# Kernel tuning notes

Measured on AMD Instinct MI355X. Metric: run time of the kernel, lower is better.

## Reference

```python
import jax, jax.numpy as jnp
import numpy as np

EMBED = 1024
HEADS = 16
HEAD_DIM = EMBED // HEADS


def setup_inputs() -> dict:
    key = jax.random.key(0)
    ks = jax.random.split(key, 8)
    N, S = 4, 2048
    scale = 1.0 / np.sqrt(HEAD_DIM)
    return {
        "values": jax.random.normal(ks[0], (N, S, EMBED), jnp.float32),
        "keys": jax.random.normal(ks[1], (N, S, EMBED), jnp.float32),
        "query": jax.random.normal(ks[2], (N, S, EMBED), jnp.float32),
        "Wv": jax.random.normal(ks[3], (HEAD_DIM, HEAD_DIM), jnp.float32) * scale,
        "Wk": jax.random.normal(ks[4], (HEAD_DIM, HEAD_DIM), jnp.float32) * scale,
        "Wq": jax.random.normal(ks[5], (HEAD_DIM, HEAD_DIM), jnp.float32) * scale,
        "Wo": jax.random.normal(ks[6], (EMBED, EMBED), jnp.float32) / np.sqrt(EMBED),
        "bo": jax.random.normal(ks[7], (EMBED,), jnp.float32) * 0.01,
    }


def reference(values, keys, query, Wv, Wk, Wq, Wo, bo):
    N = query.shape[0]
    # reshape to [N, S, H, D]
    v = values.reshape(N, -1, HEADS, HEAD_DIM)
    k = keys.reshape(N, -1, HEADS, HEAD_DIM)
    q = query.reshape(N, -1, HEADS, HEAD_DIM)
    # per-head linear projections (torch Linear: x @ W.T)
    v = jnp.einsum("nshd,ed->nshe", v, Wv)
    k = jnp.einsum("nshd,ed->nshe", k, Wk)
    q = jnp.einsum("nshd,ed->nshe", q, Wq)
    # full attention matrix [N, H, Q, K]; note scale uses embed_size**0.5 as in source
    energy = jnp.einsum("nqhd,nkhd->nhqk", q, k)
    attn = jax.nn.softmax(energy / jnp.sqrt(jnp.asarray(EMBED, energy.dtype)), axis=3)
    out = jnp.einsum("nhql,nlhd->nqhd", attn, v).reshape(N, -1, EMBED)
    return out @ Wo.T + bo
```

## Files before the change

kernel.cpp:

```cpp
#include <hip/hip_runtime.h>
#include <hip/hip_bf16.h>

#define EMBED 1024
#define HEADS 16
#define HD    64
#define NB    4
#define SEQ   2048

typedef __bf16 bf16x8 __attribute__((ext_vector_type(8)));
typedef float  f32x4  __attribute__((ext_vector_type(4)));

__device__ __forceinline__ unsigned short f2bf(float f) {
    union { float f; unsigned u; } v; v.f = f;
    unsigned r = v.u + 0x7fffu + ((v.u >> 16) & 1u);
    return (unsigned short)(r >> 16);
}

__global__ __launch_bounds__(256) void cvt_kernel(const float* __restrict__ src,
                                                  unsigned short* __restrict__ dst) {
    int i = blockIdx.x * 256 + threadIdx.x;
    float4 v = ((const float4*)src)[i];
    ushort4 o;
    o.x = f2bf(v.x); o.y = f2bf(v.y); o.z = f2bf(v.z); o.w = f2bf(v.w);
    ((ushort4*)dst)[i] = o;
}

__global__ __launch_bounds__(256) void proj_kernel(
    const float* __restrict__ xq, const float* __restrict__ xk, const float* __restrict__ xv,
    const float* __restrict__ Wq, const float* __restrict__ Wk, const float* __restrict__ Wv,
    unsigned short* __restrict__ Qp, unsigned short* __restrict__ Kp, unsigned short* __restrict__ Vt)
{
    __shared__ __align__(16) unsigned short Wl[64 * 72];
    __shared__ __align__(16) unsigned short Xl[128 * 72];

    int bx = blockIdx.x;
    int p  = bx >> 10;
    int r  = bx & 1023;
    int st = r & 15, h = (r >> 4) & 15, n = r >> 8;
    int s0 = st * 128;

    const float* x = (p == 0) ? xq : (p == 1) ? xk : xv;
    const float* W = (p == 0) ? Wq : (p == 1) ? Wk : Wv;
    const float sc = (p == 0) ? 0.045084220027780106f : 1.0f;

    int tid = threadIdx.x;

    for (int i = 0; i < 4; ++i) {
        int idx = tid + i * 256;
        int row = idx >> 4, c4 = idx & 15;
        float4 wv = ((const float4*)W)[row * 16 + c4];
        int o = row * 72 + c4 * 4;
        Wl[o] = f2bf(wv.x); Wl[o+1] = f2bf(wv.y); Wl[o+2] = f2bf(wv.z); Wl[o+3] = f2bf(wv.w);
    }
    const float* xbase = x + (size_t)(n * SEQ + s0) * EMBED + h * HD;
    for (int i = 0; i < 8; ++i) {
        int idx = tid + i * 256;
        int row = idx >> 4, c4 = idx & 15;
        float4 v = *(const float4*)(xbase + (size_t)row * EMBED + c4 * 4);
        int o = row * 72 + c4 * 4;
        Xl[o] = f2bf(v.x); Xl[o+1] = f2bf(v.y); Xl[o+2] = f2bf(v.z); Xl[o+3] = f2bf(v.w);
    }
    __syncthreads();

    int w = tid >> 6, lane = tid & 63, ln = lane & 15, qd = lane >> 4;

    bf16x8 a[2][2], b[4][2];
    for (int mt = 0; mt < 2; ++mt)
        for (int kt = 0; kt < 2; ++kt)
            a[mt][kt] = *(const bf16x8*)&Xl[(w * 32 + mt * 16 + ln) * 72 + kt * 32 + qd * 8];
    for (int nt = 0; nt < 4; ++nt)
        for (int kt = 0; kt < 2; ++kt)
            b[nt][kt] = *(const bf16x8*)&Wl[(nt * 16 + ln) * 72 + kt * 32 + qd * 8];

    f32x4 acc[2][4];
    const f32x4 fz = {0.f, 0.f, 0.f, 0.f};
    for (int mt = 0; mt < 2; ++mt) for (int nt = 0; nt < 4; ++nt) acc[mt][nt] = fz;
    for (int mt = 0; mt < 2; ++mt)
        for (int nt = 0; nt < 4; ++nt) {
            acc[mt][nt] = __builtin_amdgcn_mfma_f32_16x16x32_bf16(a[mt][0], b[nt][0], acc[mt][nt], 0, 0, 0);
            acc[mt][nt] = __builtin_amdgcn_mfma_f32_16x16x32_bf16(a[mt][1], b[nt][1], acc[mt][nt], 0, 0, 0);
        }
    __syncthreads();

    if (p < 2) {
        for (int mt = 0; mt < 2; ++mt)
            for (int nt = 0; nt < 4; ++nt)
                for (int rg = 0; rg < 4; ++rg)
                    Xl[(w * 32 + mt * 16 + qd * 4 + rg) * 72 + nt * 16 + ln] = f2bf(acc[mt][nt][rg] * sc);
        __syncthreads();
        unsigned short* outp = (p == 0 ? Qp : Kp) + (size_t)(n * HEADS + h) * SEQ * HD + (size_t)s0 * HD;
        for (int i = 0; i < 4; ++i) {
            int idx = tid + i * 256;
            int row = idx >> 3, ch = idx & 7;
            *(uint4*)(outp + (size_t)row * HD + ch * 8) = *(const uint4*)&Xl[row * 72 + ch * 8];
        }
    } else {
        for (int mt = 0; mt < 2; ++mt)
            for (int nt = 0; nt < 4; ++nt)
                for (int rg = 0; rg < 4; ++rg)
                    Xl[(nt * 16 + ln) * 136 + (w * 32 + mt * 16 + qd * 4 + rg)] = f2bf(acc[mt][nt][rg]);
        __syncthreads();
        unsigned short* outp = Vt + (size_t)(n * HEADS + h) * HD * SEQ + s0;
        for (int i = 0; i < 4; ++i) {
            int idx = tid + i * 256;
            int row = idx >> 4, ch = idx & 15;
            *(uint4*)(outp + (size_t)row * SEQ + ch * 8) = *(const uint4*)&Xl[row * 136 + ch * 8];
        }
    }
}

__global__ __launch_bounds__(256) void attn_kernel(
    const unsigned short* __restrict__ Qp, const unsigned short* __restrict__ Kp,
    const unsigned short* __restrict__ Vt, unsigned short* __restrict__ Xattn)
{
    __shared__ __align__(16) unsigned short Kl[64 * 72];
    __shared__ __align__(16) unsigned short Vl[64 * 72];
    __shared__ __align__(16) unsigned short Pl[128 * 72];

    int bx = blockIdx.x;
    int head = bx >> 4, qt = bx & 15;
    int n = head >> 4, h = head & 15;
    int q0 = qt * 128;

    int tid = threadIdx.x;
    int w = tid >> 6, lane = tid & 63, ln = lane & 15, qd = lane >> 4;

    const unsigned short* Qb = Qp + (size_t)head * SEQ * HD;
    const unsigned short* Kb = Kp + (size_t)head * SEQ * HD;
    const unsigned short* Vb = Vt + (size_t)head * HD * SEQ;

    bf16x8 qa[2][2];
    for (int mt = 0; mt < 2; ++mt)
        for (int kt = 0; kt < 2; ++kt)
            qa[mt][kt] = *(const bf16x8*)(Qb + (size_t)(q0 + w * 32 + mt * 16 + ln) * HD + kt * 32 + qd * 8);

    const f32x4 fz = {0.f, 0.f, 0.f, 0.f};
    f32x4 o[2][4];
    float lp[2][4];
    for (int mt = 0; mt < 2; ++mt)
        for (int nt = 0; nt < 4; ++nt) o[mt][nt] = fz;
    for (int mt = 0; mt < 2; ++mt)
        for (int rg = 0; rg < 4; ++rg) lp[mt][rg] = 0.f;

    int wsw = (qd & 2) << 3;
    int rsw = (ln & 8) << 1;

    for (int kc = 0; kc < SEQ; kc += 64) {
        for (int i = 0; i < 2; ++i) {
            int idx = tid + i * 256;
            int row = idx >> 3, ch = idx & 7;
            uint4 kv = *(const uint4*)(Kb + (size_t)(kc + row) * HD + ch * 8);
            uint4 vv = *(const uint4*)(Vb + (size_t)row * SEQ + kc + ch * 8);
            *(uint4*)&Kl[row * 72 + ch * 8] = kv;
            *(uint4*)&Vl[row * 72 + ch * 8] = vv;
        }
        __syncthreads();

        bf16x8 kb[4][2];
        for (int nt = 0; nt < 4; ++nt)
            for (int kt = 0; kt < 2; ++kt)
                kb[nt][kt] = *(const bf16x8*)&Kl[(nt * 16 + ln) * 72 + kt * 32 + qd * 8];
        f32x4 s[2][4];
        for (int mt = 0; mt < 2; ++mt)
            for (int nt = 0; nt < 4; ++nt) {
                f32x4 acc = fz;
                acc = __builtin_amdgcn_mfma_f32_16x16x32_bf16(qa[mt][0], kb[nt][0], acc, 0, 0, 0);
                acc = __builtin_amdgcn_mfma_f32_16x16x32_bf16(qa[mt][1], kb[nt][1], acc, 0, 0, 0);
                s[mt][nt] = acc;
            }

        for (int mt = 0; mt < 2; ++mt)
            for (int nt = 0; nt < 4; ++nt) {
                int colsw = (nt * 16 + ln) ^ wsw;
#pragma unroll
                for (int rg = 0; rg < 4; ++rg) {
                    float p = __builtin_amdgcn_exp2f(s[mt][nt][rg]);
                    lp[mt][rg] += p;
                    union { float f; unsigned u; } c; c.f = p;
                    Pl[(w * 32 + mt * 16 + qd * 4 + rg) * 72 + colsw] =
                        (unsigned short)((c.u + 0x8000u) >> 16);
                }
            }
        __asm__ volatile("s_waitcnt lgkmcnt(0)" ::: "memory");

        bf16x8 pa[2][2], vf[4][2];
        for (int mt = 0; mt < 2; ++mt)
            for (int kt = 0; kt < 2; ++kt)
                pa[mt][kt] = *(const bf16x8*)&Pl[(w * 32 + mt * 16 + ln) * 72 + ((kt * 32 + qd * 8) ^ rsw)];
        for (int nt = 0; nt < 4; ++nt)
            for (int kt = 0; kt < 2; ++kt)
                vf[nt][kt] = *(const bf16x8*)&Vl[(nt * 16 + ln) * 72 + kt * 32 + qd * 8];
        for (int mt = 0; mt < 2; ++mt)
            for (int nt = 0; nt < 4; ++nt) {
                o[mt][nt] = __builtin_amdgcn_mfma_f32_16x16x32_bf16(pa[mt][0], vf[nt][0], o[mt][nt], 0, 0, 0);
                o[mt][nt] = __builtin_amdgcn_mfma_f32_16x16x32_bf16(pa[mt][1], vf[nt][1], o[mt][nt], 0, 0, 0);
            }
        __syncthreads();
    }

    for (int mt = 0; mt < 2; ++mt)
        for (int rg = 0; rg < 4; ++rg) {
            float v = lp[mt][rg];
            for (int d = 1; d < 16; d <<= 1) v += __shfl_xor(v, d);
            lp[mt][rg] = 1.0f / v;
        }

    for (int mt = 0; mt < 2; ++mt)
        for (int nt = 0; nt < 4; ++nt)
            for (int rg = 0; rg < 4; ++rg)
                Pl[(w * 32 + mt * 16 + qd * 4 + rg) * 72 + nt * 16 + ln] = f2bf(o[mt][nt][rg] * lp[mt][rg]);
    __syncthreads();
    unsigned short* ob = Xattn + (size_t)(n * SEQ + q0) * EMBED + h * HD;
    for (int i = 0; i < 4; ++i) {
        int idx = tid + i * 256;
        int row = idx >> 3, ch = idx & 7;
        *(uint4*)(ob + (size_t)row * EMBED + ch * 8) = *(const uint4*)&Pl[row * 72 + ch * 8];
    }
}

__global__ __launch_bounds__(256) void outproj_kernel(
    const unsigned short* __restrict__ X, const unsigned short* __restrict__ Wb,
    const float* __restrict__ bo, float* __restrict__ out)
{
    __shared__ __align__(16) unsigned short Al[128 * 72];
    __shared__ __align__(16) unsigned short Bl[128 * 72];

    int bx = blockIdx.x;
    int cm = bx >> 3, cn = bx & 7;
    int m0 = cm * 128, c0 = cn * 128;
    int tid = threadIdx.x;
    int w = tid >> 6, lane = tid & 63, ln = lane & 15, qd = lane >> 4;
    int rh = (w & 1) * 64, chh = (w >> 1) * 64;

    f32x4 acc[4][4];
    const f32x4 fz = {0.f, 0.f, 0.f, 0.f};
    for (int mt = 0; mt < 4; ++mt) for (int nt = 0; nt < 4; ++nt) acc[mt][nt] = fz;

    for (int k0 = 0; k0 < EMBED; k0 += 64) {
        for (int i = 0; i < 4; ++i) {
            int idx = tid + i * 256;
            int row = idx >> 3, ch = idx & 7;
            uint4 av = *(const uint4*)(X  + (size_t)(m0 + row) * EMBED + k0 + ch * 8);
            uint4 bv = *(const uint4*)(Wb + (size_t)(c0 + row) * EMBED + k0 + ch * 8);
            *(uint4*)&Al[row * 72 + ch * 8] = av;
            *(uint4*)&Bl[row * 72 + ch * 8] = bv;
        }
        __syncthreads();
        bf16x8 af[4][2], bf_[4][2];
        for (int mt = 0; mt < 4; ++mt)
            for (int kt = 0; kt < 2; ++kt)
                af[mt][kt] = *(const bf16x8*)&Al[(rh + mt * 16 + ln) * 72 + kt * 32 + qd * 8];
        for (int nt = 0; nt < 4; ++nt)
            for (int kt = 0; kt < 2; ++kt)
                bf_[nt][kt] = *(const bf16x8*)&Bl[(chh + nt * 16 + ln) * 72 + kt * 32 + qd * 8];
        for (int mt = 0; mt < 4; ++mt)
            for (int nt = 0; nt < 4; ++nt) {
                acc[mt][nt] = __builtin_amdgcn_mfma_f32_16x16x32_bf16(af[mt][0], bf_[nt][0], acc[mt][nt], 0, 0, 0);
                acc[mt][nt] = __builtin_amdgcn_mfma_f32_16x16x32_bf16(af[mt][1], bf_[nt][1], acc[mt][nt], 0, 0, 0);
            }
        __syncthreads();
    }

    for (int nt = 0; nt < 4; ++nt) {
        int col = c0 + chh + nt * 16 + ln;
        float bias = bo[col];
        for (int mt = 0; mt < 4; ++mt) {
            int row = m0 + rh + mt * 16 + qd * 4;
            for (int rg = 0; rg < 4; ++rg)
                out[(size_t)(row + rg) * EMBED + col] = acc[mt][nt][rg] + bias;
        }
    }
}

extern "C" void kernel_launch(void* const* d_in, const int* in_sizes, int n_in,
                              void* d_out, int out_size, void* d_ws, size_t ws_size,
                              hipStream_t stream) {
    const float* values = (const float*)d_in[0];
    const float* keys   = (const float*)d_in[1];
    const float* query  = (const float*)d_in[2];
    const float* Wv     = (const float*)d_in[3];
    const float* Wk     = (const float*)d_in[4];
    const float* Wq     = (const float*)d_in[5];
    const float* Wo     = (const float*)d_in[6];
    const float* bo     = (const float*)d_in[7];
    float* out = (float*)d_out;

    unsigned short* ws = (unsigned short*)d_ws;
    const size_t HSZ = (size_t)NB * HEADS * SEQ * HD;
    unsigned short* Qp = ws;
    unsigned short* Kp = Qp + HSZ;
    unsigned short* Vt = Kp + HSZ;
    unsigned short* Xa = Vt + HSZ;
    unsigned short* Wb = Xa + HSZ;

    cvt_kernel<<<1024, 256, 0, stream>>>(Wo, Wb);
    proj_kernel<<<3072, 256, 0, stream>>>(query, keys, values, Wq, Wk, Wv, Qp, Kp, Vt);
    attn_kernel<<<1024, 256, 0, stream>>>(Qp, Kp, Vt, Xa);
    outproj_kernel<<<512, 256, 0, stream>>>(Xa, Wb, bo, out);
}
```

Before: 311.8 us.

## Double-buffer K/V and GEMM tiles, enlarge attention Q tile, compute row sums via MFMA

The attention and output-projection kernels gain register-staged double buffering of shared-memory tiles, so global loads for the next chunk overlap the MFMA work on the current one and one barrier per iteration is dropped. The attention kernel now handles 256 queries per block (64 per wave), halving the grid and reusing each K/V tile across more queries. Softmax row sums are accumulated with an MFMA against a ones vector instead of scalar adds plus a shuffle reduction. Loops are fully unrolled and launch bounds are raised, which increases register pressure and shared memory per block and may lower occupancy.

```diff
diff --git a/kernel.cpp b/kernel.cpp
--- a/kernel.cpp
+++ b/kernel.cpp
@@ -65,17 +65,26 @@
     int w = tid >> 6, lane = tid & 63, ln = lane & 15, qd = lane >> 4;
 
     bf16x8 a[2][2], b[4][2];
+#pragma unroll
     for (int mt = 0; mt < 2; ++mt)
+#pragma unroll
         for (int kt = 0; kt < 2; ++kt)
             a[mt][kt] = *(const bf16x8*)&Xl[(w * 32 + mt * 16 + ln) * 72 + kt * 32 + qd * 8];
+#pragma unroll
     for (int nt = 0; nt < 4; ++nt)
+#pragma unroll
         for (int kt = 0; kt < 2; ++kt)
             b[nt][kt] = *(const bf16x8*)&Wl[(nt * 16 + ln) * 72 + kt * 32 + qd * 8];
 
     f32x4 acc[2][4];
     const f32x4 fz = {0.f, 0.f, 0.f, 0.f};
-    for (int mt = 0; mt < 2; ++mt) for (int nt = 0; nt < 4; ++nt) acc[mt][nt] = fz;
+#pragma unroll
     for (int mt = 0; mt < 2; ++mt)
+#pragma unroll
+        for (int nt = 0; nt < 4; ++nt) acc[mt][nt] = fz;
+#pragma unroll
+    for (int mt = 0; mt < 2; ++mt)
+#pragma unroll
         for (int nt = 0; nt < 4; ++nt) {
             acc[mt][nt] = __builtin_amdgcn_mfma_f32_16x16x32_bf16(a[mt][0], b[nt][0], acc[mt][nt], 0, 0, 0);
             acc[mt][nt] = __builtin_amdgcn_mfma_f32_16x16x32_bf16(a[mt][1], b[nt][1], acc[mt][nt], 0, 0, 0);
@@ -83,8 +92,11 @@
     __syncthreads();
 
     if (p < 2) {
+#pragma unroll
         for (int mt = 0; mt < 2; ++mt)
+#pragma unroll
             for (int nt = 0; nt < 4; ++nt)
+#pragma unroll
                 for (int rg = 0; rg < 4; ++rg)
                     Xl[(w * 32 + mt * 16 + qd * 4 + rg) * 72 + nt * 16 + ln] = f2bf(acc[mt][nt][rg] * sc);
         __syncthreads();
@@ -95,8 +107,11 @@
             *(uint4*)(outp + (size_t)row * HD + ch * 8) = *(const uint4*)&Xl[row * 72 + ch * 8];
         }
     } else {
+#pragma unroll
         for (int mt = 0; mt < 2; ++mt)
+#pragma unroll
             for (int nt = 0; nt < 4; ++nt)
+#pragma unroll
                 for (int rg = 0; rg < 4; ++rg)
                     Xl[(nt * 16 + ln) * 136 + (w * 32 + mt * 16 + qd * 4 + rg)] = f2bf(acc[mt][nt][rg]);
         __syncthreads();
@@ -109,18 +124,18 @@
     }
 }
 
-__global__ __launch_bounds__(256) void attn_kernel(
+__global__ __launch_bounds__(256, 2) void attn_kernel(
     const unsigned short* __restrict__ Qp, const unsigned short* __restrict__ Kp,
     const unsigned short* __restrict__ Vt, unsigned short* __restrict__ Xattn)
 {
-    __shared__ __align__(16) unsigned short Kl[64 * 72];
-    __shared__ __align__(16) unsigned short Vl[64 * 72];
-    __shared__ __align__(16) unsigned short Pl[128 * 72];
+    __shared__ __align__(16) unsigned short Kl[2][64 * 72];
+    __shared__ __align__(16) unsigned short Vl[2][64 * 72];
+    __shared__ __align__(16) unsigned short Pl[256 * 72];
 
     int bx = blockIdx.x;
-    int head = bx >> 4, qt = bx & 15;
+    int head = bx >> 3, qt = bx & 7;
     int n = head >> 4, h = head & 15;
-    int q0 = qt * 128;
+    int q0 = qt * 256;
 
     int tid = threadIdx.x;
     int w = tid >> 6, lane = tid & 63, ln = lane & 15, qd = lane >> 4;
@@ -129,101 +144,161 @@
     const unsigned short* Kb = Kp + (size_t)head * SEQ * HD;
     const unsigned short* Vb = Vt + (size_t)head * HD * SEQ;
 
-    bf16x8 qa[2][2];
-    for (int mt = 0; mt < 2; ++mt)
+    bf16x8 qa[4][2];
+#pragma unroll
+    for (int mt = 0; mt < 4; ++mt)
+#pragma unroll
         for (int kt = 0; kt < 2; ++kt)
-            qa[mt][kt] = *(const bf16x8*)(Qb + (size_t)(q0 + w * 32 + mt * 16 + ln) * HD + kt * 32 + qd * 8);
+            qa[mt][kt] = *(const bf16x8*)(Qb + (size_t)(q0 + w * 64 + mt * 16 + ln) * HD + kt * 32 + qd * 8);
 
     const f32x4 fz = {0.f, 0.f, 0.f, 0.f};
-    f32x4 o[2][4];
-    float lp[2][4];
-    for (int mt = 0; mt < 2; ++mt)
+    f32x4 o[4][4], l4[4];
+#pragma unroll
+    for (int mt = 0; mt < 4; ++mt) {
+        l4[mt] = fz;
+#pragma unroll
         for (int nt = 0; nt < 4; ++nt) o[mt][nt] = fz;
-    for (int mt = 0; mt < 2; ++mt)
-        for (int rg = 0; rg < 4; ++rg) lp[mt][rg] = 0.f;
-
+    }
+
+    bf16x8 ones;
+    {
+        union { short s[8]; bf16x8 v; } uo;
+#pragma unroll
+        for (int i = 0; i < 8; ++i) uo.s[i] = 0x3F80;
+        ones = uo.v;
+    }
+
+    int srow = tid >> 3, sch = tid & 7;
     int wsw = (qd & 2) << 3;
     int rsw = (ln & 8) << 1;
 
+    uint4 rK[2], rV[2];
+#pragma unroll
+    for (int i = 0; i < 2; ++i) {
+        int row = srow + i * 32;
+        rK[i] = *(const uint4*)(Kb + (size_t)row * HD + sch * 8);
+        rV[i] = *(const uint4*)(Vb + (size_t)row * SEQ + 0 + sch * 8);
+    }
+#pragma unroll
+    for (int i = 0; i < 2; ++i) {
+        int row = srow + i * 32;
+        *(uint4*)&Kl[0][row * 72 + sch * 8] = rK[i];
+        *(uint4*)&Vl[0][row * 72 + sch * 8] = rV[i];
+    }
+#pragma unroll
+    for (int i = 0; i < 2; ++i) {
+        int row = srow + i * 32;
+        rK[i] = *(const uint4*)(Kb + (size_t)(64 + row) * HD + sch * 8);
+        rV[i] = *(const uint4*)(Vb + (size_t)row * SEQ + 64 + sch * 8);
+    }
+
     for (int kc = 0; kc < SEQ; kc += 64) {
-        for (int i = 0; i < 2; ++i) {
-            int idx = tid + i * 256;
-            int row = idx >> 3, ch = idx & 7;
-            uint4 kv = *(const uint4*)(Kb + (size_t)(kc + row) * HD + ch * 8);
-            uint4 vv = *(const uint4*)(Vb + (size_t)row * SEQ + kc + ch * 8);
-            *(uint4*)&Kl[row * 72 + ch * 8] = kv;
-            *(uint4*)&Vl[row * 72 + ch * 8] = vv;
-        }
+        int cur = (kc >> 6) & 1, nxt = cur ^ 1;
         __syncthreads();
 
+        if (kc + 64 < SEQ) {
+#pragma unroll
+            for (int i = 0; i < 2; ++i) {
+                int row = srow + i * 32;
+                *(uint4*)&Kl[nxt][row * 72 + sch * 8] = rK[i];
+                *(uint4*)&Vl[nxt][row * 72 + sch * 8] = rV[i];
+            }
+            int kn = kc + 128 <= SEQ - 64 ? kc + 128 : SEQ - 64;
+#pragma unroll
+            for (int i = 0; i < 2; ++i) {
+                int row = srow + i * 32;
+                rK[i] = *(const uint4*)(Kb + (size_t)(kn + row) * HD + sch * 8);
+                rV[i] = *(const uint4*)(Vb + (size_t)row * SEQ + kn + sch * 8);
+            }
+        }
+
         bf16x8 kb[4][2];
+#pragma unroll
         for (int nt = 0; nt < 4; ++nt)
+#pragma unroll
             for (int kt = 0; kt < 2; ++kt)
-                kb[nt][kt] = *(const bf16x8*)&Kl[(nt * 16 + ln) * 72 + kt * 32 + qd * 8];
-        f32x4 s[2][4];
-        for (int mt = 0; mt < 2; ++mt)
-            for (int nt = 0; nt < 4; ++nt) {
-                f32x4 acc = fz;
-                acc = __builtin_amdgcn_mfma_f32_16x16x32_bf16(qa[mt][0], kb[nt][0], acc, 0, 0, 0);
-                acc = __builtin_amdgcn_mfma_f32_16x16x32_bf16(qa[mt][1], kb[nt][1], acc, 0, 0, 0);
-                s[mt][nt] = acc;
-            }
-
-        for (int mt = 0; mt < 2; ++mt)
-            for (int nt = 0; nt < 4; ++nt) {
-                int colsw = (nt * 16 + ln) ^ wsw;
-#pragma unroll
-                for (int rg = 0; rg < 4; ++rg) {
-                    float p = __builtin_amdgcn_exp2f(s[mt][nt][rg]);
-                    lp[mt][rg] += p;
-                    union { float f; unsigned u; } c; c.f = p;
-                    Pl[(w * 32 + mt * 16 + qd * 4 + rg) * 72 + colsw] =
-                        (unsigned short)((c.u + 0x8000u) >> 16);
+                kb[nt][kt] = *(const bf16x8*)&Kl[cur][(nt * 16 + ln) * 72 + kt * 32 + qd * 8];
+
+#pragma unroll
+        for (int mh = 0; mh < 2; ++mh) {
+            f32x4 s[2][4];
+#pragma unroll
+            for (int m2 = 0; m2 < 2; ++m2)
+#pragma unroll
+                for (int nt = 0; nt < 4; ++nt) {
+                    int mt = mh * 2 + m2;
+                    f32x4 acc = fz;
+                    acc = __builtin_amdgcn_mfma_f32_16x16x32_bf16(qa[mt][0], kb[nt][0], acc, 0, 0, 0);
+                    acc = __builtin_amdgcn_mfma_f32_16x16x32_bf16(qa[mt][1], kb[nt][1], acc, 0, 0, 0);
+                    s[m2][nt] = acc;
                 }
-            }
+#pragma unroll
+            for (int m2 = 0; m2 < 2; ++m2)
+#pragma unroll
+                for (int nt = 0; nt < 4; ++nt) {
+                    int mt = mh * 2 + m2;
+                    int colsw = (nt * 16 + ln) ^ wsw;
+#pragma unroll
+                    for (int rg = 0; rg < 4; ++rg) {
+                        float p = __builtin_amdgcn_exp2f(s[m2][nt][rg]);
+                        union { float f; unsigned u; } c; c.f = p;
+                        Pl[(w * 64 + mt * 16 + qd * 4 + rg) * 72 + colsw] =
+                            (unsigned short)((c.u + 0x8000u) >> 16);
+                    }
+                }
+        }
         __asm__ volatile("s_waitcnt lgkmcnt(0)" ::: "memory");
 
-        bf16x8 pa[2][2], vf[4][2];
-        for (int mt = 0; mt < 2; ++mt)
+        bf16x8 pa[4][2], vf[4][2];
+#pragma unroll
+        for (int mt = 0; mt < 4; ++mt)
+#pragma unroll
             for (int kt = 0; kt < 2; ++kt)
-                pa[mt][kt] = *(const bf16x8*)&Pl[(w * 32 + mt * 16 + ln) * 72 + ((kt * 32 + qd * 8) ^ rsw)];
+                pa[mt][kt] = *(const bf16x8*)&Pl[(w * 64 + mt * 16 + ln) * 72 + ((kt * 32 + qd * 8) ^ rsw)];
+#pragma unroll
         for (int nt = 0; nt < 4; ++nt)
+#pragma unroll
             for (int kt = 0; kt < 2; ++kt)
-                vf[nt][kt] = *(const bf16x8*)&Vl[(nt * 16 + ln) * 72 + kt * 32 + qd * 8];
-        for (int mt = 0; mt < 2; ++mt)
+                vf[nt][kt] = *(const bf16x8*)&Vl[cur][(nt * 16 + ln) * 72 + kt * 32 + qd * 8];
+#pragma unroll
+        for (int mt = 0; mt < 4; ++mt) {
+            l4[mt] = __builtin_amdgcn_mfma_f32_16x16x32_bf16(pa[mt][0], ones, l4[mt], 0, 0, 0);
+            l4[mt] = __builtin_amdgcn_mfma_f32_16x16x32_bf16(pa[mt][1], ones, l4[mt], 0, 0, 0);
+#pragma unroll
             for (int nt = 0; nt < 4; ++nt) {
                 o[mt][nt] = __builtin_amdgcn_mfma_f32_16x16x32_bf16(pa[mt][0], vf[nt][0], o[mt][nt], 0, 0, 0);
                 o[mt][nt] = __builtin_amdgcn_mfma_f32_16x16x32_bf16(pa[mt][1], vf[nt][1], o[mt][nt], 0, 0, 0);
             }
-        __syncthreads();
-    }
-
-    for (int mt = 0; mt < 2; ++mt)
-        for (int rg = 0; rg < 4; ++rg) {
-            float v = lp[mt][rg];
-            for (int d = 1; d < 16; d <<= 1) v += __shfl_xor(v, d);
-            lp[mt][rg] = 1.0f / v;
-        }
-
-    for (int mt = 0; mt < 2; ++mt)
+        }
+    }
+
+    __syncthreads();
+#pragma unroll
+    for (int mt = 0; mt < 4; ++mt) {
+        float inv[4];
+#pragma unroll
+        for (int rg = 0; rg < 4; ++rg) inv[rg] = 1.0f / l4[mt][rg];
+#pragma unroll
         for (int nt = 0; nt < 4; ++nt)
+#pragma unroll
             for (int rg = 0; rg < 4; ++rg)
-                Pl[(w * 32 + mt * 16 + qd * 4 + rg) * 72 + nt * 16 + ln] = f2bf(o[mt][nt][rg] * lp[mt][rg]);
+                Pl[(w * 64 + mt * 16 + qd * 4 + rg) * 72 + nt * 16 + ln] = f2bf(o[mt][nt][rg] * inv[rg]);
+    }
     __syncthreads();
     unsigned short* ob = Xattn + (size_t)(n * SEQ + q0) * EMBED + h * HD;
-    for (int i = 0; i < 4; ++i) {
+    for (int i = 0; i < 8; ++i) {
         int idx = tid + i * 256;
         int row = idx >> 3, ch = idx & 7;
         *(uint4*)(ob + (size_t)row * EMBED + ch * 8) = *(const uint4*)&Pl[row * 72 + ch * 8];
     }
 }
 
-__global__ __launch_bounds__(256) void outproj_kernel(
+__global__ __launch_bounds__(256, 2) void outproj_kernel(
     const unsigned short* __restrict__ X, const unsigned short* __restrict__ Wb,
     const float* __restrict__ bo, float* __restrict__ out)
 {
-    __shared__ __align__(16) unsigned short Al[128 * 72];
-    __shared__ __align__(16) unsigned short Bl[128 * 72];
+    __shared__ __align__(16) unsigned short Al[2][128 * 72];
+    __shared__ __align__(16) unsigned short Bl[2][128 * 72];
 
     int bx = blockIdx.x;
     int cm = bx >> 3, cn = bx & 7;
@@ -234,38 +309,76 @@
 
     f32x4 acc[4][4];
     const f32x4 fz = {0.f, 0.f, 0.f, 0.f};
-    for (int mt = 0; mt < 4; ++mt) for (int nt = 0; nt < 4; ++nt) acc[mt][nt] = fz;
+#pragma unroll
+    for (int mt = 0; mt < 4; ++mt)
+#pragma unroll
+        for (int nt = 0; nt < 4; ++nt) acc[mt][nt] = fz;
+
+    int srow = tid >> 1, sch = tid & 1;
+
+    uint4 rA[4], rB[4];
+#pragma unroll
+    for (int i = 0; i < 4; ++i) {
+        rA[i] = *(const uint4*)(X  + (size_t)(m0 + srow) * EMBED + 0 + (sch * 4 + i) * 8);
+        rB[i] = *(const uint4*)(Wb + (size_t)(c0 + srow) * EMBED + 0 + (sch * 4 + i) * 8);
+    }
+#pragma unroll
+    for (int i = 0; i < 4; ++i) {
+        *(uint4*)&Al[0][srow * 72 + (sch * 4 + i) * 8] = rA[i];
+        *(uint4*)&Bl[0][srow * 72 + (sch * 4 + i) * 8] = rB[i];
+    }
+#pragma unroll
+    for (int i = 0; i < 4; ++i) {
+        rA[i] = *(const uint4*)(X  + (size_t)(m0 + srow) * EMBED + 64 + (sch * 4 + i) * 8);
+        rB[i] = *(const uint4*)(Wb + (size_t)(c0 + srow) * EMBED + 64 + (sch * 4 + i) * 8);
+    }
 
     for (int k0 = 0; k0 < EMBED; k0 += 64) {
-        for (int i = 0; i < 4; ++i) {
-            int idx = tid + i * 256;
-            int row = idx >> 3, ch = idx & 7;
-            uint4 av = *(const uint4*)(X  + (size_t)(m0 + row) * EMBED + k0 + ch * 8);
-            uint4 bv = *(const uint4*)(Wb + (size_t)(c0 + row) * EMBED + k0 + ch * 8);
-            *(uint4*)&Al[row * 72 + ch * 8] = av;
-            *(uint4*)&Bl[row * 72 + ch * 8] = bv;
-        }
+        int cur = (k0 >> 6) & 1, nxt = cur ^ 1;
         __syncthreads();
+
+        if (k0 + 64 < EMBED) {
+#pragma unroll
+            for (int i = 0; i < 4; ++i) {
+                *(uint4*)&Al[nxt][srow * 72 + (sch * 4 + i) * 8] = rA[i];
+                *(uint4*)&Bl[nxt][srow * 72 + (sch * 4 + i) * 8] = rB[i];
+            }
+            int kn = k0 + 128 <= EMBED - 64 ? k0 + 128 : EMBED - 64;
+#pragma unroll
+            for (int i = 0; i < 4; ++i) {
+                rA[i] = *(const uint4*)(X  + (size_t)(m0 + srow) * EMBED + kn + (sch * 4 + i) * 8);
+                rB[i] = *(const uint4*)(Wb + (size_t)(c0 + srow) * EMBED + kn + (sch * 4 + i) * 8);
+            }
+        }
+
         bf16x8 af[4][2], bf_[4][2];
+#pragma unroll
         for (int mt = 0; mt < 4; ++mt)
+#pragma unroll
             for (int kt = 0; kt < 2; ++kt)
-                af[mt][kt] = *(const bf16x8*)&Al[(rh + mt * 16 + ln) * 72 + kt * 32 + qd * 8];
+                af[mt][kt] = *(const bf16x8*)&Al[cur][(rh + mt * 16 + ln) * 72 + kt * 32 + qd * 8];
+#pragma unroll
         for (int nt = 0; nt < 4; ++nt)
+#pragma unroll
             for (int kt = 0; kt < 2; ++kt)
-                bf_[nt][kt] = *(const bf16x8*)&Bl[(chh + nt * 16 + ln) * 72 + kt * 32 + qd * 8];
+                bf_[nt][kt] = *(const bf16x8*)&Bl[cur][(chh + nt * 16 + ln) * 72 + kt * 32 + qd * 8];
+#pragma unroll
         for (int mt = 0; mt < 4; ++mt)
+#pragma unroll
             for (int nt = 0; nt < 4; ++nt) {
                 acc[mt][nt] = __builtin_amdgcn_mfma_f32_16x16x32_bf16(af[mt][0], bf_[nt][0], acc[mt][nt], 0, 0, 0);
                 acc[mt][nt] = __builtin_amdgcn_mfma_f32_16x16x32_bf16(af[mt][1], bf_[nt][1], acc[mt][nt], 0, 0, 0);
             }
-        __syncthreads();
-    }
-
+    }
+
+#pragma unroll
     for (int nt = 0; nt < 4; ++nt) {
         int col = c0 + chh + nt * 16 + ln;
         float bias = bo[col];
+#pragma unroll
         for (int mt = 0; mt < 4; ++mt) {
             int row = m0 + rh + mt * 16 + qd * 4;
+#pragma unroll
             for (int rg = 0; rg < 4; ++rg)
                 out[(size_t)(row + rg) * EMBED + col] = acc[mt][nt][rg] + bias;
         }
@@ -295,6 +408,6 @@
 
     cvt_kernel<<<1024, 256, 0, stream>>>(Wo, Wb);
     proj_kernel<<<3072, 256, 0, stream>>>(query, keys, values, Wq, Wk, Wv, Qp, Kp, Vt);
-    attn_kernel<<<1024, 256, 0, stream>>>(Qp, Kp, Vt, Xa);
+    attn_kernel<<<512, 256, 0, stream>>>(Qp, Kp, Vt, Xa);
     outproj_kernel<<<512, 256, 0, stream>>>(Xa, Wb, bo, out);
 }
```

Measured after the change: 354.3 us. 13.7% more time.
